# Kernel optimization log

Hardware: AMD Instinct MI355X
Metric: run time of the kernel (lower is better)

Reference implementation:

```python
import jax, jax.numpy as jnp
import numpy as np

EMBED_DIM = 1024
NUM_HEADS = 16
CONTEXT = 250
MAX_PERIOD = 10000.0
HEAD_DIM = EMBED_DIM // NUM_HEADS


def setup_inputs() -> dict:
    key = jax.random.key(0)
    k1, k2, k3 = jax.random.split(key, 3)
    B, T = 2, 2048
    query = jax.random.normal(k1, (B, T, EMBED_DIM), jnp.float32)
    in_proj_w = jax.random.normal(k2, (3 * EMBED_DIM, EMBED_DIM), jnp.float32) * (EMBED_DIM ** -0.5)
    out_proj_w = jax.random.normal(k3, (EMBED_DIM, EMBED_DIM), jnp.float32) * (EMBED_DIM ** -0.5)
    return {"query": query, "in_proj_w": in_proj_w, "out_proj_w": out_proj_w}


def _apply_rope(q, k):
    # q, k: [B, H, T, D]; Mimi/Moshi-style interleaved-pair rotary embedding
    B, H, T, D = q.shape
    ds = jnp.arange(D // 2, dtype=jnp.float32)
    freqs = jnp.exp(ds * (-np.log(MAX_PERIOD) * 2.0 / D))  # [D/2]
    ts = jnp.arange(T, dtype=jnp.float32)
    ang = ts[:, None] * freqs[None, :]  # [T, D/2]
    cos = jnp.cos(ang)
    sin = jnp.sin(ang)

    def rot(x):
        xr = x.reshape(B, H, T, D // 2, 2)
        xa, xb = xr[..., 0], xr[..., 1]
        ya = xa * cos - xb * sin
        yb = xa * sin + xb * cos
        return jnp.stack([ya, yb], axis=-1).reshape(B, H, T, D)

    return rot(q), rot(k)


def reference(query, in_proj_w, out_proj_w):
    B, T, E = query.shape
    H, D = NUM_HEADS, HEAD_DIM
    # fused QKV projection (no bias)
    proj = query @ in_proj_w.T  # [B, T, 3E]
    qkv = proj.reshape(B, T, 3, H, D)
    q = jnp.transpose(qkv[:, :, 0], (0, 2, 1, 3))  # [B, H, T, D]
    k = jnp.transpose(qkv[:, :, 1], (0, 2, 1, 3))
    v = jnp.transpose(qkv[:, :, 2], (0, 2, 1, 3))
    q, k = _apply_rope(q, k)
    # causal sliding-window mask: attend iff 0 <= (t_q - t_k) < CONTEXT
    pos = jnp.arange(T)
    delta = pos[:, None] - pos[None, :]  # [T, T]
    mask = (delta >= 0) & (delta < CONTEXT)
    scores = jnp.einsum('bhtd,bhsd->bhts', q, k) * (D ** -0.5)
    scores = jnp.where(mask[None, None, :, :], scores, jnp.finfo(scores.dtype).min)
    attn = jax.nn.softmax(scores, axis=-1)
    x = jnp.einsum('bhts,bhsd->bhtd', attn, v)  # [B, H, T, D]
    x = jnp.transpose(x, (0, 2, 1, 3)).reshape(B, T, E)
    return x @ out_proj_w.T
```

## Files before the change

### kernel.cpp

```cpp
#include <hip/hip_runtime.h>

#define TT 2048
#define EMB 1024
#define NH 16
#define HD 64
#define CTX 250

typedef __attribute__((ext_vector_type(4))) float f32x4;
typedef __attribute__((ext_vector_type(8))) short s16x8;
typedef __attribute__((ext_vector_type(4))) short s16x4;

#define LDS_PTR(p) ((__attribute__((address_space(3))) void*)(p))
#define GLB_PTR(p) ((const __attribute__((address_space(1))) void*)(p))

__device__ __forceinline__ short f2bf(float f) {
  union { float f; unsigned u; } v; v.f = f;
  unsigned r = v.u + 0x7fffu + ((v.u >> 16) & 1u);
  return (short)(r >> 16);
}
__device__ __forceinline__ float bf2f(unsigned short u) {
  union { unsigned u; float f; } v; v.u = ((unsigned)u) << 16;
  return v.f;
}

__global__ void cvt_all(const float* __restrict__ q, const float* __restrict__ wi,
                        const float* __restrict__ wo, short* __restrict__ qo,
                        short* __restrict__ wio, short* __restrict__ woo,
                        float2* __restrict__ tbl) {
  int i = blockIdx.x * blockDim.x + threadIdx.x;
  if (i >= 2097152) {
    int tix = (i - 2097152) * 4;
#pragma unroll
    for (int e = 0; e < 4; ++e) {
      int idx = tix + e;
      int t = idx >> 5, fi = idx & 31;
      float freq = __expf(-(float)fi * 0.2878231366f);
      float s, c;
      sincosf((float)t * freq, &s, &c);
      tbl[idx] = make_float2(c, s);
    }
    return;
  }
  const float* src; short* dst; int off;
  if (i < 1048576)      { src = q;  dst = qo;  off = i; }
  else if (i < 1835008) { src = wi; dst = wio; off = i - 1048576; }
  else                  { src = wo; dst = woo; off = i - 1835008; }
  float4 v = reinterpret_cast<const float4*>(src)[off];
  s16x4 o; o[0] = f2bf(v.x); o[1] = f2bf(v.y); o[2] = f2bf(v.z); o[3] = f2bf(v.w);
  *reinterpret_cast<s16x4*>(dst + off * 4) = o;
}

__global__ __launch_bounds__(512) void gemm_qkv(const short* __restrict__ A,
                                                const short* __restrict__ W,
                                                short* __restrict__ Qb,
                                                short* __restrict__ Kb,
                                                short* __restrict__ Vt,
                                                const float2* __restrict__ tbl,
                                                int N, int K) {
  constexpr int BM = 128, BK = 32, MFR = 2;
  __shared__ __align__(16) short As[BM * BK];
  __shared__ __align__(16) short Bs[128 * BK];
  const int lane = threadIdx.x & 63;
  const int wid  = threadIdx.x >> 6;
  const int lr = lane & 15, lg = lane >> 4;
  const int xcd = blockIdx.x & 7;
  const int sub = blockIdx.x >> 3;
  const int bx = (sub % 12) + 12 * (xcd & 1);
  const int by = (sub / 12) + 8 * (xcd >> 1);
  const int rblk = by * BM;
  const int cblk = bx * 128;
  const int wrow = (wid >> 1) * 32;
  const int wcol = (wid & 1) * 64;
  const int sel = cblk >> 10;
  const int lrow = lane >> 2;
  const int fst  = (lrow & 3) ^ ((lrow >> 2) & 3);
  const int schunk = ((lane & 3) ^ fst) * 8;
  const int frd = (lr & 3) ^ ((lr >> 2) & 3);
  const int rd_off = lr * 32 + ((lg ^ frd) * 8);
  const int p = wid * 16 + lrow;
  const int prow = (sel < 2) ? ((p & 64) + 2 * (p & 31) + ((p >> 5) & 1)) : p;
  const short* Abase = A + (size_t)(rblk + p) * K + schunk;
  const short* Wbase = W + (size_t)(cblk + prow) * K + schunk;
  f32x4 acc[MFR][4] = {};

  for (int kk = 0; kk < K; kk += BK) {
    __builtin_amdgcn_global_load_lds(GLB_PTR(Abase + kk), LDS_PTR(&As[wid * 512]), 16, 0, 0);
    __builtin_amdgcn_global_load_lds(GLB_PTR(Wbase + kk), LDS_PTR(&Bs[wid * 512]), 16, 0, 0);
    __syncthreads();
    s16x8 af[MFR], bfr[4];
#pragma unroll
    for (int m = 0; m < MFR; m++)
      af[m] = *reinterpret_cast<const s16x8*>(&As[((wid >> 1) * 2 + m) * 512 + rd_off]);
#pragma unroll
    for (int n = 0; n < 4; n++)
      bfr[n] = *reinterpret_cast<const s16x8*>(&Bs[((wid & 1) * 4 + n) * 512 + rd_off]);
#pragma unroll
    for (int m = 0; m < MFR; m++)
#pragma unroll
      for (int n = 0; n < 4; n++)
        acc[m][n] = __builtin_amdgcn_mfma_f32_16x16x32_bf16(af[m], bfr[n], acc[m][n], 0, 0, 0);
    __syncthreads();
  }

  if (sel == 2) {
    const int dcol_base = (cblk & 1023) + wcol;
#pragma unroll
    for (int m = 0; m < MFR; m++) {
      int trow = rblk + wrow + m * 16 + lg * 4;
      int b = trow >> 11;
      int tq = trow & 2047;
#pragma unroll
      for (int n = 0; n < 4; n++) {
        int dcol = dcol_base + n * 16 + lr;
        int h = dcol >> 6;
        int d = dcol & 63;
        size_t bh = (size_t)(b * NH + h);
        s16x4 pk;
#pragma unroll
        for (int r = 0; r < 4; r++) pk[r] = f2bf(acc[m][n][r]);
        *reinterpret_cast<s16x4*>(Vt + (bh * HD + d) * TT + tq) = pk;
      }
    }
  } else {
    short* dst = (sel == 0) ? Qb : Kb;
    const int h = ((cblk & 1023) + wcol) >> 6;
#pragma unroll
    for (int m = 0; m < MFR; m++) {
      int trow = rblk + wrow + m * 16 + lg * 4;
      int b = trow >> 11;
      int tq = trow & 2047;
      size_t bh = (size_t)(b * NH + h);
#pragma unroll
      for (int n = 0; n < 2; n++) {
        int i = n * 16 + lr;
        const float2* tp = tbl + (size_t)tq * 32 + i;
#pragma unroll
        for (int r = 0; r < 4; r++) {
          float xa = acc[m][n][r];
          float xb = acc[m][n + 2][r];
          float2 cs = tp[r * 32];
          float ya = xa * cs.x - xb * cs.y;
          float yb = xa * cs.y + xb * cs.x;
          unsigned pk = ((unsigned)(unsigned short)f2bf(yb) << 16) |
                        (unsigned short)f2bf(ya);
          *reinterpret_cast<unsigned*>(dst + (bh * TT + tq + r) * HD + 2 * i) = pk;
        }
      }
    }
  }
}

template<int BM, int LX, int LY, bool BF16OUT>
__global__ __launch_bounds__(256) void gemm_swz(const short* __restrict__ A,
                                                const short* __restrict__ W,
                                                void* __restrict__ Cv, int N, int K) {
  constexpr int BK = 32;
  constexpr int MFR = BM / 32;
  __shared__ __align__(16) short As[BM * BK];
  __shared__ __align__(16) short Bs[128 * BK];
  const int lane = threadIdx.x & 63;
  const int wid  = threadIdx.x >> 6;
  const int lr = lane & 15, lg = lane >> 4;
  const int xcd = blockIdx.x & 7;
  const int sub = blockIdx.x >> 3;
  const int bx = (sub % LX) + LX * (xcd & 1);
  const int by = (sub / LX) + LY * (xcd >> 1);
  const int rblk = by * BM;
  const int cblk = bx * 128;
  const int wrow = (wid >> 1) * (BM / 2);
  const int wcol = (wid & 1) * 64;
  const int srow = lane >> 2;
  const int scol = (lane & 3) * 8;
  f32x4 acc[MFR][4] = {};

  for (int kk = 0; kk < K; kk += BK) {
#pragma unroll
    for (int j = 0; j < BM / 64; j++) {
      int seg = wid * (BM / 64) + j;
      const short* g = A + (size_t)(rblk + seg * 16 + srow) * K + kk + scol;
      __builtin_amdgcn_global_load_lds(GLB_PTR(g), LDS_PTR(&As[seg * 512]), 16, 0, 0);
    }
#pragma unroll
    for (int j = 0; j < 2; j++) {
      int seg = wid * 2 + j;
      const short* g = W + (size_t)(cblk + seg * 16 + srow) * K + kk + scol;
      __builtin_amdgcn_global_load_lds(GLB_PTR(g), LDS_PTR(&Bs[seg * 512]), 16, 0, 0);
    }
    __syncthreads();
    s16x8 af[MFR], bfr[4];
#pragma unroll
    for (int m = 0; m < MFR; m++)
      af[m] = *reinterpret_cast<const s16x8*>(&As[(wrow + m * 16 + lr) * BK + lg * 8]);
#pragma unroll
    for (int n = 0; n < 4; n++)
      bfr[n] = *reinterpret_cast<const s16x8*>(&Bs[(wcol + n * 16 + lr) * BK + lg * 8]);
#pragma unroll
    for (int m = 0; m < MFR; m++)
#pragma unroll
      for (int n = 0; n < 4; n++)
        acc[m][n] = __builtin_amdgcn_mfma_f32_16x16x32_bf16(af[m], bfr[n], acc[m][n], 0, 0, 0);
    __syncthreads();
  }
#pragma unroll
  for (int m = 0; m < MFR; m++)
#pragma unroll
    for (int n = 0; n < 4; n++)
#pragma unroll
      for (int r = 0; r < 4; r++) {
        int row = rblk + wrow + m * 16 + lg * 4 + r;
        int col = cblk + wcol + n * 16 + lr;
        float val = acc[m][n][r];
        if constexpr (BF16OUT) ((short*)Cv)[(size_t)row * N + col] = f2bf(val);
        else                   ((float*)Cv)[(size_t)row * N + col] = val;
      }
}

__global__ __launch_bounds__(256) void attn_v4(const short* __restrict__ Qb,
                                               const short* __restrict__ Kb,
                                               const short* __restrict__ Vt,
                                               short* __restrict__ Xout) {
  int tid = threadIdx.x;
  int lane = tid & 63;
  int w = tid >> 6;
  int lr = lane & 15, lg = lane >> 4;
  int id = blockIdx.x;
  int xcd = id & 7;
  int sub = id >> 3;
  int bh = xcd * 4 + (sub >> 5);
  int tblk = (sub & 31) * 64;
  int t0 = tblk + w * 16;
  int b = bh >> 4, h = bh & 15;
  const short* Qp = Qb + bh * TT * HD;
  const char* Kp = (const char*)(Kb + bh * TT * HD);
  const char* Vtp = (const char*)(Vt + bh * HD * TT);
  __shared__ __align__(16) short Ks[32 * 64];
  __shared__ __align__(16) short Vs[64 * 32];
  __shared__ __align__(16) short p_lds[4][16][40];
  s16x8 qf[2];
#pragma unroll
  for (int d2 = 0; d2 < 2; d2++)
    qf[d2] = *reinterpret_cast<const s16x8*>(Qp + (t0 + lr) * HD + d2 * 32 + lg * 8);
  s16x8 ones;
#pragma unroll
  for (int j = 0; j < 8; j++) ones[j] = (short)0x3F80;
  f32x4 of[4] = {};
  f32x4 ofl = {};
  int lo = tblk - (CTX - 1); if (lo < 0) lo = 0;
  int kt_lo = lo & ~31;
  int kt_hi = (tblk + 63) & ~31;
  int krow = w * 8 + (lane >> 3);
  int kcb  = ((lane & 7) * 16) ^ ((krow & 7) << 4);
  int vd   = w * 16 + (lane >> 2);
  int vcb  = ((lane & 3) * 16) ^ (((vd >> 1) & 3) << 4);
  char* ksdst = (char*)Ks + w * 1024 + lane * 16;
  char* vsdst = (char*)Vs + w * 1024 + lane * 16;
  for (int kt = kt_lo; kt <= kt_hi; kt += 32) {
    __builtin_amdgcn_global_load_lds(GLB_PTR(Kp + (kt + krow) * 128 + kcb),
                                     LDS_PTR(ksdst), 16, 0, 0);
    __builtin_amdgcn_global_load_lds(GLB_PTR(Vtp + vd * (TT * 2) + kt * 2 + vcb),
                                     LDS_PTR(vsdst), 16, 0, 0);
    __syncthreads();
    if (kt <= t0 + 15 && kt + 31 >= t0 - (CTX - 1)) {
      f32x4 s2[2];
#pragma unroll
      for (int hh = 0; hh < 2; hh++) {
        int row = hh * 16 + lr;
        f32x4 sa = {};
#pragma unroll
        for (int d2 = 0; d2 < 2; d2++) {
          int cb = (d2 * 64 + lg * 16) ^ ((row & 7) << 4);
          s16x8 kf = *reinterpret_cast<const s16x8*>((const char*)Ks + row * 128 + cb);
          sa = __builtin_amdgcn_mfma_f32_16x16x32_bf16(qf[d2], kf, sa, 0, 0, 0);
        }
        s2[hh] = sa;
      }
#pragma unroll
      for (int r = 0; r < 4; r++) {
        int row = t0 + lg * 4 + r;
#pragma unroll
        for (int hh = 0; hh < 2; hh++) {
          int col = kt + hh * 16 + lr;
          int dl = row - col;
          bool vdm = (dl >= 0) && (dl < CTX);
          float pv = vdm ? __expf(s2[hh][r] * 0.125f) : 0.0f;
          p_lds[w][lg * 4 + r][hh * 16 + lr] = f2bf(pv);
        }
      }
      s16x8 pa = *reinterpret_cast<const s16x8*>(&p_lds[w][lr][lg * 8]);
#pragma unroll
      for (int n = 0; n < 4; n++) {
        int d = n * 16 + lr;
        int cb = (lg * 16) ^ (((d >> 1) & 3) << 4);
        s16x8 vf = *reinterpret_cast<const s16x8*>((const char*)Vs + d * 64 + cb);
        of[n] = __builtin_amdgcn_mfma_f32_16x16x32_bf16(pa, vf, of[n], 0, 0, 0);
      }
      ofl = __builtin_amdgcn_mfma_f32_16x16x32_bf16(pa, ones, ofl, 0, 0, 0);
    }
    __syncthreads();
  }
#pragma unroll
  for (int r = 0; r < 4; r++) {
    float inv = 1.0f / ofl[r];
    int row = t0 + lg * 4 + r;
#pragma unroll
    for (int n = 0; n < 4; n++)
      Xout[(b * TT + row) * EMB + h * HD + n * 16 + lr] = f2bf(of[n][r] * inv);
  }
}

extern "C" void kernel_launch(void* const* d_in, const int* in_sizes, int n_in,
                              void* d_out, int out_size, void* d_ws, size_t ws_size,
                              hipStream_t stream) {
  const float* query = (const float*)d_in[0];
  const float* w_in  = (const float*)d_in[1];
  const float* w_out = (const float*)d_in[2];
  char* ws = (char*)d_ws;
  short* qbf   = (short*)(ws + 0);
  short* wibf  = (short*)(ws + 8388608);
  short* wobf  = (short*)(ws + 14680064);
  float2* tbl  = (float2*)(ws + 16777216);
  short* attnx = (short*)(ws + 17301504);
  short* Qb    = (short*)(ws + 41943040);
  short* Kb    = (short*)(ws + 50331648);
  short* Vt    = (short*)(ws + 58720256);

  cvt_all<<<8256, 256, 0, stream>>>(query, w_in, w_out, qbf, wibf, wobf, tbl);
  gemm_qkv<<<768, 512, 0, stream>>>(qbf, wibf, Qb, Kb, Vt, tbl, 3072, 1024);
  attn_v4<<<1024, 256, 0, stream>>>(Qb, Kb, Vt, attnx);
  gemm_swz<64, 4, 16, false><<<512, 256, 0, stream>>>(attnx, wobf, d_out, 1024, 1024);
}
```

Baseline: 86.49 us.

## Double QKV GEMM K-tile and rewrite output GEMM with 8 waves and swizzled LDS

The QKV projection GEMM now stages a 64-wide K slice per barrier pair instead of 32, running two MFMA sub-steps per sync. This halves the number of barriers and doubles LDS use. The output projection GEMM is replaced by a 512-thread kernel where each of 8 waves computes a 16x64 tile. It uses the XOR-swizzled LDS layout from the QKV kernel, which should cut bank conflicts and add per-block parallelism for latency hiding. Only half the waves load A, which leaves their load slots unused.

```diff
diff --git a/kernel.cpp b/kernel.cpp
--- a/kernel.cpp
+++ b/kernel.cpp
@@ -57,7 +57,7 @@
                                                 short* __restrict__ Vt,
                                                 const float2* __restrict__ tbl,
                                                 int N, int K) {
-  constexpr int BM = 128, BK = 32, MFR = 2;
+  constexpr int BM = 128, BK = 64, MFR = 2;
   __shared__ __align__(16) short As[BM * BK];
   __shared__ __align__(16) short Bs[128 * BK];
   const int lane = threadIdx.x & 63;
@@ -84,21 +84,31 @@
   f32x4 acc[MFR][4] = {};
 
   for (int kk = 0; kk < K; kk += BK) {
-    __builtin_amdgcn_global_load_lds(GLB_PTR(Abase + kk), LDS_PTR(&As[wid * 512]), 16, 0, 0);
-    __builtin_amdgcn_global_load_lds(GLB_PTR(Wbase + kk), LDS_PTR(&Bs[wid * 512]), 16, 0, 0);
-    __syncthreads();
-    s16x8 af[MFR], bfr[4];
-#pragma unroll
-    for (int m = 0; m < MFR; m++)
-      af[m] = *reinterpret_cast<const s16x8*>(&As[((wid >> 1) * 2 + m) * 512 + rd_off]);
-#pragma unroll
-    for (int n = 0; n < 4; n++)
-      bfr[n] = *reinterpret_cast<const s16x8*>(&Bs[((wid & 1) * 4 + n) * 512 + rd_off]);
-#pragma unroll
-    for (int m = 0; m < MFR; m++)
+#pragma unroll
+    for (int h = 0; h < 2; h++) {
+      __builtin_amdgcn_global_load_lds(GLB_PTR(Abase + kk + h * 32),
+                                       LDS_PTR(&As[(wid * 2 + h) * 512]), 16, 0, 0);
+      __builtin_amdgcn_global_load_lds(GLB_PTR(Wbase + kk + h * 32),
+                                       LDS_PTR(&Bs[(wid * 2 + h) * 512]), 16, 0, 0);
+    }
+    __syncthreads();
+#pragma unroll
+    for (int kh = 0; kh < 2; kh++) {
+      s16x8 af[MFR], bfr[4];
+#pragma unroll
+      for (int m = 0; m < MFR; m++)
+        af[m] = *reinterpret_cast<const s16x8*>(
+            &As[(((wid >> 1) * 2 + m) * 2 + kh) * 512 + rd_off]);
 #pragma unroll
       for (int n = 0; n < 4; n++)
-        acc[m][n] = __builtin_amdgcn_mfma_f32_16x16x32_bf16(af[m], bfr[n], acc[m][n], 0, 0, 0);
+        bfr[n] = *reinterpret_cast<const s16x8*>(
+            &Bs[(((wid & 1) * 4 + n) * 2 + kh) * 512 + rd_off]);
+#pragma unroll
+      for (int m = 0; m < MFR; m++)
+#pragma unroll
+        for (int n = 0; n < 4; n++)
+          acc[m][n] = __builtin_amdgcn_mfma_f32_16x16x32_bf16(af[m], bfr[n], acc[m][n], 0, 0, 0);
+    }
     __syncthreads();
   }
 
@@ -150,12 +160,10 @@
   }
 }
 
-template<int BM, int LX, int LY, bool BF16OUT>
-__global__ __launch_bounds__(256) void gemm_swz(const short* __restrict__ A,
-                                                const short* __restrict__ W,
-                                                void* __restrict__ Cv, int N, int K) {
-  constexpr int BK = 32;
-  constexpr int MFR = BM / 32;
+__global__ __launch_bounds__(512) void gemm_out8(const short* __restrict__ A,
+                                                 const short* __restrict__ W,
+                                                 float* __restrict__ C, int N, int K) {
+  constexpr int BM = 64, BK = 32;
   __shared__ __align__(16) short As[BM * BK];
   __shared__ __align__(16) short Bs[128 * BK];
   const int lane = threadIdx.x & 63;
@@ -163,56 +171,44 @@
   const int lr = lane & 15, lg = lane >> 4;
   const int xcd = blockIdx.x & 7;
   const int sub = blockIdx.x >> 3;
-  const int bx = (sub % LX) + LX * (xcd & 1);
-  const int by = (sub / LX) + LY * (xcd >> 1);
+  const int bx = (sub % 4) + 4 * (xcd & 1);
+  const int by = (sub / 4) + 16 * (xcd >> 1);
   const int rblk = by * BM;
   const int cblk = bx * 128;
-  const int wrow = (wid >> 1) * (BM / 2);
-  const int wcol = (wid & 1) * 64;
-  const int srow = lane >> 2;
-  const int scol = (lane & 3) * 8;
-  f32x4 acc[MFR][4] = {};
+  const int wm = wid >> 1;
+  const int wn = wid & 1;
+  const int lrow = lane >> 2;
+  const int fst  = (lrow & 3) ^ ((lrow >> 2) & 3);
+  const int schunk = ((lane & 3) ^ fst) * 8;
+  const int frd = (lr & 3) ^ ((lr >> 2) & 3);
+  const int rd_off = lr * 32 + ((lg ^ frd) * 8);
+  const short* Abase = A + (size_t)(rblk + wid * 16 + lrow) * K + schunk;
+  const short* Wbase = W + (size_t)(cblk + wid * 16 + lrow) * K + schunk;
+  f32x4 acc[4] = {};
 
   for (int kk = 0; kk < K; kk += BK) {
-#pragma unroll
-    for (int j = 0; j < BM / 64; j++) {
-      int seg = wid * (BM / 64) + j;
-      const short* g = A + (size_t)(rblk + seg * 16 + srow) * K + kk + scol;
-      __builtin_amdgcn_global_load_lds(GLB_PTR(g), LDS_PTR(&As[seg * 512]), 16, 0, 0);
-    }
-#pragma unroll
-    for (int j = 0; j < 2; j++) {
-      int seg = wid * 2 + j;
-      const short* g = W + (size_t)(cblk + seg * 16 + srow) * K + kk + scol;
-      __builtin_amdgcn_global_load_lds(GLB_PTR(g), LDS_PTR(&Bs[seg * 512]), 16, 0, 0);
-    }
-    __syncthreads();
-    s16x8 af[MFR], bfr[4];
-#pragma unroll
-    for (int m = 0; m < MFR; m++)
-      af[m] = *reinterpret_cast<const s16x8*>(&As[(wrow + m * 16 + lr) * BK + lg * 8]);
+    if (wid < 4)
+      __builtin_amdgcn_global_load_lds(GLB_PTR(Abase + kk), LDS_PTR(&As[wid * 512]), 16, 0, 0);
+    __builtin_amdgcn_global_load_lds(GLB_PTR(Wbase + kk), LDS_PTR(&Bs[wid * 512]), 16, 0, 0);
+    __syncthreads();
+    s16x8 af, bfr[4];
+    af = *reinterpret_cast<const s16x8*>(&As[wm * 512 + rd_off]);
 #pragma unroll
     for (int n = 0; n < 4; n++)
-      bfr[n] = *reinterpret_cast<const s16x8*>(&Bs[(wcol + n * 16 + lr) * BK + lg * 8]);
-#pragma unroll
-    for (int m = 0; m < MFR; m++)
-#pragma unroll
-      for (int n = 0; n < 4; n++)
-        acc[m][n] = __builtin_amdgcn_mfma_f32_16x16x32_bf16(af[m], bfr[n], acc[m][n], 0, 0, 0);
-    __syncthreads();
-  }
-#pragma unroll
-  for (int m = 0; m < MFR; m++)
+      bfr[n] = *reinterpret_cast<const s16x8*>(&Bs[(wn * 4 + n) * 512 + rd_off]);
 #pragma unroll
     for (int n = 0; n < 4; n++)
-#pragma unroll
-      for (int r = 0; r < 4; r++) {
-        int row = rblk + wrow + m * 16 + lg * 4 + r;
-        int col = cblk + wcol + n * 16 + lr;
-        float val = acc[m][n][r];
-        if constexpr (BF16OUT) ((short*)Cv)[(size_t)row * N + col] = f2bf(val);
-        else                   ((float*)Cv)[(size_t)row * N + col] = val;
-      }
+      acc[n] = __builtin_amdgcn_mfma_f32_16x16x32_bf16(af, bfr[n], acc[n], 0, 0, 0);
+    __syncthreads();
+  }
+#pragma unroll
+  for (int n = 0; n < 4; n++)
+#pragma unroll
+    for (int r = 0; r < 4; r++) {
+      int row = rblk + wm * 16 + lg * 4 + r;
+      int col = cblk + wn * 64 + n * 16 + lr;
+      C[(size_t)row * N + col] = acc[n][r];
+    }
 }
 
 __global__ __launch_bounds__(256) void attn_v4(const short* __restrict__ Qb,
@@ -327,5 +323,5 @@
   cvt_all<<<8256, 256, 0, stream>>>(query, w_in, w_out, qbf, wibf, wobf, tbl);
   gemm_qkv<<<768, 512, 0, stream>>>(qbf, wibf, Qb, Kb, Vt, tbl, 3072, 1024);
   attn_v4<<<1024, 256, 0, stream>>>(Qb, Kb, Vt, attnx);
-  gemm_swz<64, 4, 16, false><<<512, 256, 0, stream>>>(attnx, wobf, d_out, 1024, 1024);
-}
+  gemm_out8<<<512, 512, 0, stream>>>(attnx, wobf, (float*)d_out, 1024, 1024);
+}
```

Result: no change. 85.79 us (-0.8%).
